# Optimization experiments

Hardware: AMD Instinct MI355X
Metric: run time of the kernel (lower is better)

## Reference

```python
import jax, jax.numpy as jnp
import numpy as np

NUM_HEADS = 12
EPS = 1e-5


def _pool_norm(t, w, g, b, thw, stride):
    # t: [B, heads, 1+L, hd]. Depthwise Conv3d pooling on non-cls tokens, then LayerNorm(hd).
    B, Hn, _, hd = t.shape
    cls, body = t[:, :, :1], t[:, :, 1:]
    T, Hs, Ws = thw
    x = body.reshape(B * Hn, T, Hs, Ws, hd).transpose(0, 4, 1, 2, 3)  # [B*heads, hd, T, H, W]
    pad = [(w.shape[2] // 2,) * 2, (w.shape[3] // 2,) * 2, (w.shape[4] // 2,) * 2]
    y = jax.lax.conv_general_dilated(x, w, window_strides=stride, padding=pad,
                                     feature_group_count=hd,
                                     dimension_numbers=('NCDHW', 'OIDHW', 'NCDHW'))
    Tp, Hp, Wp = y.shape[2], y.shape[3], y.shape[4]
    y = y.reshape(B, Hn, hd, Tp * Hp * Wp).transpose(0, 1, 3, 2)  # [B, heads, Lp, hd]
    y = jnp.concatenate([cls, y], axis=2)
    mu = y.mean(-1, keepdims=True)
    var = ((y - mu) ** 2).mean(-1, keepdims=True)
    return (y - mu) * jax.lax.rsqrt(var + EPS) * g + b


def _forward(x, Wq, Wk, Wv, Wproj, b_proj, pq, pk, pv, gq, bq, gk, bk, gv, bv, thw):
    B, N, C = x.shape
    hd = C // NUM_HEADS
    def proj(W):
        return (x @ W.T).reshape(B, N, NUM_HEADS, hd).transpose(0, 2, 1, 3)  # [B, heads, N, hd]
    q = _pool_norm(proj(Wq), pq, gq, bq, thw, (1, 2, 2))
    k = _pool_norm(proj(Wk), pk, gk, bk, thw, (1, 4, 4))
    v = _pool_norm(proj(Wv), pv, gv, bv, thw, (1, 4, 4))
    scale = hd ** -0.5
    attn = jax.nn.softmax(jnp.einsum('bhqd,bhkd->bhqk', q * scale, k), axis=-1)
    o = jnp.einsum('bhqk,bhkd->bhqd', attn, v)
    o = o.transpose(0, 2, 1, 3).reshape(B, o.shape[2], C)
    return o @ Wproj.T + b_proj


def setup_inputs() -> dict:
    key = jax.random.key(0)
    ks = jax.random.split(key, 8)
    B, T, H, W, C = 8, 8, 28, 28, 768
    hd = C // NUM_HEADS
    N = T * H * W + 1  # cls token
    s = lambda k, sh: jax.random.normal(k, sh, jnp.float32) * 0.02
    return {
        'x': jax.random.normal(ks[0], (B, N, C), jnp.float32),
        'Wq': s(ks[1], (C, C)), 'Wk': s(ks[2], (C, C)), 'Wv': s(ks[3], (C, C)),
        'Wproj': s(ks[4], (C, C)), 'b_proj': jnp.zeros((C,), jnp.float32),
        'pool_q_w': s(ks[5], (hd, 1, 3, 3, 3)),
        'pool_k_w': s(ks[6], (hd, 1, 3, 3, 3)),
        'pool_v_w': s(ks[7], (hd, 1, 3, 3, 3)),
        'gq': jnp.ones((hd,), jnp.float32), 'bq': jnp.zeros((hd,), jnp.float32),
        'gk': jnp.ones((hd,), jnp.float32), 'bk': jnp.zeros((hd,), jnp.float32),
        'gv': jnp.ones((hd,), jnp.float32), 'bv': jnp.zeros((hd,), jnp.float32),
        'thw_t': 8, 'thw_h': 28, 'thw_w': 28,
    }


def reference(x, Wq, Wk, Wv, Wproj, b_proj, pool_q_w, pool_k_w, pool_v_w,
              gq, bq, gk, bk, gv, bv, thw_t, thw_h, thw_w):
    return _forward(x, Wq, Wk, Wv, Wproj, b_proj, pool_q_w, pool_k_w, pool_v_w,
                    gq, bq, gk, bk, gv, bv, (thw_t, thw_h, thw_w))
```

## Files before the change

kernel.cpp:

```cpp
#include <hip/hip_runtime.h>

using bf16   = __bf16;
using bf16x4 = __attribute__((ext_vector_type(4))) __bf16;
using bf16x8 = __attribute__((ext_vector_type(8))) __bf16;
using f32x4  = __attribute__((ext_vector_type(4))) float;
using u32x4  = __attribute__((ext_vector_type(4))) unsigned int;

#define MFMA16(a,b,c) __builtin_amdgcn_mfma_f32_16x16x32_bf16((a),(b),(c),0,0,0)

__device__ inline void glds16(const void* g, void* l) {
    __builtin_amdgcn_global_load_lds(
        (__attribute__((address_space(1))) void*)(const_cast<void*>(g)),
        (__attribute__((address_space(3))) void*)(l), 16, 0, 0);
}

__device__ inline int xcd_remap(int bid, int nwg) {
    const int xcd = bid & 7, loc = bid >> 3;
    const int q8 = nwg >> 3, r8 = nwg & 7;
    return (xcd < r8 ? xcd * (q8 + 1) : r8 * (q8 + 1) + (xcd - r8) * q8) + loc;
}

constexpr int CB   = 8;
constexpr int NH   = 12;
constexpr int CC   = 768;
constexpr int HD   = 64;
constexpr int TT   = 8, HH = 28, WW = 28;
constexpr int NTOK = TT*HH*WW + 1;
constexpr int MX   = CB*NTOK;
constexpr int MXP  = 50304;
constexpr int NQ   = 1569, NQP = 1600;
constexpr int NK   = 393,  NKP = 416;
constexpr int MO   = CB*NQ;
constexpr int MOP  = 12672;
constexpr int CTOK = 1 + TT*20*20;
constexpr int MKV  = CB*CTOK;
constexpr int MKVP = 25856;

__global__ __launch_bounds__(256) void prep_all(const float* __restrict__ x,
                                                const float* __restrict__ Wq, const float* __restrict__ Wk,
                                                const float* __restrict__ Wv, const float* __restrict__ Wp,
                                                const float* __restrict__ pqw, const float* __restrict__ pkw,
                                                const float* __restrict__ pvw,
                                                const float* __restrict__ gq, const float* __restrict__ bq,
                                                const float* __restrict__ gk, const float* __restrict__ bk,
                                                bf16* __restrict__ xb, bf16* __restrict__ wdst,
                                                float* __restrict__ wt, float* __restrict__ Mb) {
    constexpr int WSZ = 589824;
    const int bid = blockIdx.x, tid = threadIdx.x;
    if (bid < 4096) {
        const int nvalid = MX * CC, ntotal = MXP * CC;
        int i = (bid * 256 + tid) * 4;
        const int stride = 4096 * 256 * 4;
        for (; i < ntotal; i += stride) {
            bf16x4 o;
            if (i + 3 < nvalid) {
                f32x4 v = *(const f32x4*)(x + i);
                #pragma unroll
                for (int e = 0; e < 4; ++e) o[e] = (bf16)v[e];
            } else {
                #pragma unroll
                for (int e = 0; e < 4; ++e) {
                    int k = i + e;
                    o[e] = (bf16)((k < nvalid) ? x[k] : 0.f);
                }
            }
            *(bf16x4*)(xb + i) = o;
        }
    } else if (bid < 6400) {
        int i = ((bid - 4096) * 256 + tid) * 4;
        const int setn = i / WSZ, j = i % WSZ;
        const float* src = (setn == 0) ? Wq : (setn == 1) ? Wk : (setn == 2) ? Wv : Wp;
        f32x4 v = *(const f32x4*)(src + j);
        bf16x4 o;
        #pragma unroll
        for (int e = 0; e < 4; ++e) o[e] = (bf16)v[e];
        *(bf16x4*)(wdst + i) = o;
    } else if (bid < 6421) {
        int i = (bid - 6400) * 256 + tid;
        if (i < 3 * 1728) {
            int setn = i / 1728, j = i % 1728;
            const float* src = (setn == 0) ? pqw : (setn == 1) ? pkw : pvw;
            int tap = j / 64, c = j % 64;
            wt[i] = src[c * 27 + tap];
        }
    } else if (tid < 64) {
        const int c = tid;
        float mgq = fabsf(gq[c]), sbq = bq[c] * bq[c];
        float mgk = fabsf(gk[c]), sbk = bk[c] * bk[c];
        #pragma unroll
        for (int m = 1; m < 64; m <<= 1) {
            mgq = fmaxf(mgq, __shfl_xor(mgq, m)); sbq += __shfl_xor(sbq, m);
            mgk = fmaxf(mgk, __shfl_xor(mgk, m)); sbk += __shfl_xor(sbk, m);
        }
        if (c == 0) {
            const float Bq = 8.f * mgq + sqrtf(sbq);
            const float Bk = 8.f * mgk + sqrtf(sbk);
            Mb[0] = 0.125f * Bq * Bk;
        }
    }
}

__global__ __launch_bounds__(512, 2) void gemmU(const bf16* __restrict__ xb,
                                                const bf16* __restrict__ wqkv,
                                                bf16* __restrict__ tmpq,
                                                bf16* __restrict__ tmpkv) {
    extern __shared__ char lds[];
    const int wgid = xcd_remap(blockIdx.x, gridDim.x);

    const int tid = threadIdx.x, lane = tid & 63, w = tid >> 6;
    const int li = lane & 15, lg = lane >> 4;
    const int wr = w >> 2, wc = w & 3;
    const int lr  = lane >> 3;
    const int lsw = ((lane & 7) ^ lr) << 3;

    const bool isQ = wgid < 591;
    int bm, bn, Mv, ldc;
    const bf16* Bb;
    bf16* C;
    if (isQ) { bm = wgid / 3;        bn = wgid % 3;        Mv = MXP;  ldc = 768;
               Bb = wqkv + (size_t)bn * 256 * 768;               C = tmpq; }
    else     { int t = wgid - 591;   bm = t / 6; bn = t % 6; Mv = MKVP; ldc = 1536;
               Bb = wqkv + (size_t)(768 + bn * 256) * 768;       C = tmpkv; }

    const bf16* abase[4];
    const bf16* bbase[4];
    #pragma unroll
    for (int h_ = 0; h_ < 4; ++h_) {
        int gr = bm * 256 + h_ * 64 + w * 8 + lr;
        size_t orig;
        if (isQ) {
            if (gr > MXP - 1) gr = MXP - 1;
            orig = (size_t)gr;
        } else {
            if (gr > MKV - 1) gr = MKV - 1;
            const unsigned b = (unsigned)gr / 3201u;
            const unsigned p = (unsigned)gr % 3201u;
            if (p == 0) orig = (size_t)b * NTOK;
            else {
                const unsigned q  = p - 1;
                const unsigned t2 = q / 400u, rem = q % 400u;
                const unsigned hi = rem / 20u, wi = rem % 20u;
                const int ih = 4 * (int)((hi + 1) / 3) + (int)((hi + 1) % 3) - 1;
                const int iw = 4 * (int)((wi + 1) / 3) + (int)((wi + 1) % 3) - 1;
                orig = (size_t)b * NTOK + 1 + ((size_t)t2 * HH + ih) * WW + iw;
            }
        }
        abase[h_] = xb + orig * 768 + lsw;
        bbase[h_] = Bb + (size_t)(h_ * 64 + w * 8 + lr) * 768 + lsw;
    }

    const int sw_  = (li & 7) << 4;
    const int swc0 = (lg * 16) ^ sw_;
    const int swc1 = (64 | (lg * 16)) ^ sw_;

#define STAGE_T(Tt, buf) do {                                                        \
        char* d_ = lds + (buf) * 65536;                                              \
        _Pragma("unroll")                                                            \
        for (int h_ = 0; h_ < 4; ++h_)                                               \
            glds16(abase[h_] + (size_t)(Tt) * 64, d_ + (h_ * 64 + w * 8) * 128);     \
        _Pragma("unroll")                                                            \
        for (int h_ = 0; h_ < 4; ++h_)                                               \
            glds16(bbase[h_] + (size_t)(Tt) * 64, d_ + 32768 + (h_ * 64 + w * 8) * 128); \
    } while (0)

    f32x4 acc[8][4] = {};
    bf16x8 aF[8], bF[4];

#define READ_K(sw)                                                                   \
    _Pragma("unroll") for (int mf = 0; mf < 8; ++mf)                                 \
        aF[mf] = *(const bf16x8*)(bufA + (size_t)(wr * 128 + mf * 16 + li) * 128 + (sw)); \
    _Pragma("unroll") for (int nf = 0; nf < 4; ++nf)                                 \
        bF[nf] = *(const bf16x8*)(bufB + (size_t)(wc * 64 + nf * 16 + li) * 128 + (sw));

#define MFMA_K()                                                                     \
    _Pragma("unroll") for (int mf = 0; mf < 8; ++mf)                                 \
    _Pragma("unroll") for (int nf = 0; nf < 4; ++nf)                                 \
        acc[mf][nf] = MFMA16(aF[mf], bF[nf], acc[mf][nf]);

    STAGE_T(0, 0);
    STAGE_T(1, 1);
    asm volatile("s_waitcnt vmcnt(8)" ::: "memory");
    __builtin_amdgcn_s_barrier();
    __builtin_amdgcn_sched_barrier(0);

    #pragma unroll
    for (int T = 0; T < 12; ++T) {
        const char* bufA = lds + (T & 1) * 65536;
        const char* bufB = bufA + 32768;
        if (T >= 1 && T < 11) STAGE_T(T + 1, (T + 1) & 1);
        READ_K(swc0);
        __builtin_amdgcn_s_setprio(1);
        MFMA_K();
        __builtin_amdgcn_s_setprio(0);
        READ_K(swc1);
        __builtin_amdgcn_s_setprio(1);
        MFMA_K();
        __builtin_amdgcn_s_setprio(0);
        asm volatile("s_waitcnt lgkmcnt(0)" ::: "memory");
        if (T < 11) asm volatile("s_waitcnt vmcnt(0)" ::: "memory");
        __builtin_amdgcn_s_barrier();
        __builtin_amdgcn_sched_barrier(0);
    }
#undef STAGE_T
#undef READ_K
#undef MFMA_K

    #pragma unroll
    for (int mf = 0; mf < 8; ++mf) {
        const int row0 = bm * 256 + wr * 128 + mf * 16 + lg * 4;
        #pragma unroll
        for (int nf = 0; nf < 4; ++nf) {
            const int col = bn * 256 + wc * 64 + nf * 16 + li;
            #pragma unroll
            for (int r = 0; r < 4; ++r) {
                const int row = row0 + r;
                if (row < Mv)
                    C[(size_t)row * ldc + col] = (bf16)acc[mf][nf][r];
            }
        }
    }
}

__global__ __launch_bounds__(512, 2) void gemmF(const bf16* __restrict__ A,
                                                const bf16* __restrict__ Bw,
                                                float* __restrict__ Cptr,
                                                const float* __restrict__ bias,
                                                int nbn, int Mvalid, int Aclamp) {
    extern __shared__ char lds[];
    const int wgid = xcd_remap(blockIdx.x, gridDim.x);
    const int bm = wgid / nbn, bn = wgid % nbn;

    const int tid = threadIdx.x, lane = tid & 63, w = tid >> 6;
    const int li = lane & 15, lg = lane >> 4;
    const int wr = w >> 2, wc = w & 3;
    const int lr  = lane >> 3;
    const int lsw = ((lane & 7) ^ lr) << 3;
    const bf16* Agp = A  + (size_t)bm * 256 * 768;
    const bf16* Bgp = Bw + (size_t)bn * 128 * 768;
    const int clampA = Aclamp - bm * 256;

    const int sw_  = (li & 7) << 4;
    const int swc0 = (lg * 16) ^ sw_;
    const int swc1 = (64 | (lg * 16)) ^ sw_;

#define STAGE_T(Tt, buf) do {                                                        \
        char* d_ = lds + (buf) * 49152;                                              \
        _Pragma("unroll")                                                            \
        for (int h_ = 0; h_ < 4; ++h_) {                                             \
            const int r0_ = h_ * 64 + w * 8;                                         \
            int gr_ = r0_ + lr; if (gr_ >= clampA) gr_ = clampA - 1;                 \
            glds16(Agp + (size_t)gr_ * 768 + (Tt) * 64 + lsw, d_ + r0_ * 128);       \
        }                                                                            \
        _Pragma("unroll")                                                            \
        for (int h_ = 0; h_ < 2; ++h_) {                                             \
            const int r0_ = h_ * 64 + w * 8;                                         \
            glds16(Bgp + (size_t)(r0_ + lr) * 768 + (Tt) * 64 + lsw,                 \
                   d_ + 32768 + r0_ * 128);                                          \
        } } while (0)

    f32x4 acc[8][2] = {};
    bf16x8 aF[8], bF[2];

#define READ_K(sw)                                                                   \
    _Pragma("unroll") for (int mf = 0; mf < 8; ++mf)                                 \
        aF[mf] = *(const bf16x8*)(bufA + (size_t)(wr * 128 + mf * 16 + li) * 128 + (sw)); \
    _Pragma("unroll") for (int nf = 0; nf < 2; ++nf)                                 \
        bF[nf] = *(const bf16x8*)(bufB + (size_t)(wc * 32 + nf * 16 + li) * 128 + (sw));

#define MFMA_K()                                                                     \
    _Pragma("unroll") for (int mf = 0; mf < 8; ++mf)                                 \
    _Pragma("unroll") for (int nf = 0; nf < 2; ++nf)                                 \
        acc[mf][nf] = MFMA16(aF[mf], bF[nf], acc[mf][nf]);

    STAGE_T(0, 0);
    STAGE_T(1, 1);
    asm volatile("s_waitcnt vmcnt(6)" ::: "memory");
    __builtin_amdgcn_s_barrier();
    __builtin_amdgcn_sched_barrier(0);

    #pragma unroll
    for (int T = 0; T < 12; ++T) {
        const char* bufA = lds + (T & 1) * 49152;
        const char* bufB = bufA + 32768;
        if (T >= 1 && T < 11) STAGE_T(T + 1, (T + 1) & 1);
        READ_K(swc0);
        __builtin_amdgcn_s_setprio(1);
        MFMA_K();
        __builtin_amdgcn_s_setprio(0);
        READ_K(swc1);
        __builtin_amdgcn_s_setprio(1);
        MFMA_K();
        __builtin_amdgcn_s_setprio(0);
        asm volatile("s_waitcnt lgkmcnt(0)" ::: "memory");
        if (T < 11) asm volatile("s_waitcnt vmcnt(0)" ::: "memory");
        __builtin_amdgcn_s_barrier();
        __builtin_amdgcn_sched_barrier(0);
    }
#undef STAGE_T
#undef READ_K
#undef MFMA_K

    #pragma unroll
    for (int mf = 0; mf < 8; ++mf) {
        const int row0 = bm * 256 + wr * 128 + mf * 16 + lg * 4;
        #pragma unroll
        for (int nf = 0; nf < 2; ++nf) {
            const int col = bn * 128 + wc * 32 + nf * 16 + li;
            #pragma unroll
            for (int r = 0; r < 4; ++r) {
                const int row = row0 + r;
                if (row < Mvalid)
                    Cptr[(size_t)row * 768 + col] = acc[mf][nf][r] + bias[col];
            }
        }
    }
}

__device__ __forceinline__ void pool_q4(int gw, int lane,
                                        const bf16* __restrict__ P,
                                        const float* __restrict__ wt,
                                        const float* __restrict__ gamma,
                                        const float* __restrict__ beta,
                                        bf16* __restrict__ outp) {
    constexpr int TASKS = 57;
    const int bh = gw / TASKS, task = gw % TASKS;
    const int b = bh / NH, head = bh % NH;
    const int owp = lane >> 3, cg = lane & 7, c = cg * 8;
    const size_t pbase = (size_t)b * NTOK * 768 + head * HD + c;

    if (task == TASKS - 1) {
        if (owp == 0) {
            bf16x8 v = *(const bf16x8*)(P + pbase);
            float a[8];
            #pragma unroll
            for (int e = 0; e < 8; ++e) a[e] = (float)v[e];
            float s = 0;
            #pragma unroll
            for (int e = 0; e < 8; ++e) s += a[e];
            s += __shfl_xor(s, 1); s += __shfl_xor(s, 2); s += __shfl_xor(s, 4);
            const float mu = s * 0.015625f;
            float v2 = 0;
            #pragma unroll
            for (int e = 0; e < 8; ++e) { float d = a[e] - mu; v2 += d * d; }
            v2 += __shfl_xor(v2, 1); v2 += __shfl_xor(v2, 2); v2 += __shfl_xor(v2, 4);
            const float rs = rsqrtf(v2 * 0.015625f + 1e-5f);
            f32x4 g0 = *(const f32x4*)(gamma + c), g1 = *(const f32x4*)(gamma + c + 4);
            f32x4 b0 = *(const f32x4*)(beta + c),  b1 = *(const f32x4*)(beta + c + 4);
            bf16x8 o;
            #pragma unroll
            for (int e = 0; e < 4; ++e) {
                o[e]     = (bf16)(((a[e]     - mu) * rs * g0[e] + b0[e]) * 0.125f);
                o[4 + e] = (bf16)(((a[4 + e] - mu) * rs * g1[e] + b1[e]) * 0.125f);
            }
            *(bf16x8*)(outp + ((size_t)bh * NQP) * HD + c) = o;
        } else {
            bf16x8 z = {};
            for (int p = NQ + owp - 1; p < NQP; p += 7)
                *(bf16x8*)(outp + ((size_t)bh * NQP + p) * HD + c) = z;
        }
        return;
    }

    const int tp = task / 14, oh = task % 14;
    const bool active = (owp < 7);

    float a00[8] = {}, a01[8] = {}, a10[8] = {}, a11[8] = {};
    #pragma unroll
    for (int pl = 0; pl < 4; ++pl) {
        const int it = 2 * tp - 1 + pl;
        if (it < 0 || it >= TT) continue;
        #pragma unroll
        for (int dh = 0; dh < 3; ++dh) {
            const int ih = 2 * oh + dh - 1;
            if (ih < 0 || ih >= HH) continue;
            const int rowh = 1 + (it * HH + ih) * WW;
            #pragma unroll
            for (int du = 0; du < 5; ++du) {
                const int iw = 4 * owp - 1 + du;
                if (active && iw >= 0 && iw < WW) {
                    bf16x8 v = *(const bf16x8*)(P + pbase + (size_t)(rowh + iw) * 768);
                    float fv[8];
                    #pragma unroll
                    for (int e = 0; e < 8; ++e) fv[e] = (float)v[e];
#define TAP(ACC, DT, DW) do {                                                        \
        const float* wp_ = wt + (((DT) * 3 + dh) * 3 + (DW)) * 64 + c;               \
        f32x4 w0_ = *(const f32x4*)wp_, w1_ = *(const f32x4*)(wp_ + 4);              \
        _Pragma("unroll")                                                            \
        for (int e = 0; e < 4; ++e) {                                                \
            ACC[e]     += w0_[e] * fv[e];                                            \
            ACC[4 + e] += w1_[e] * fv[4 + e];                                        \
        } } while (0)
                    if (du <= 2) {
                        if (pl <= 2) TAP(a00, pl,     du);
                        if (pl >= 1) TAP(a10, pl - 1, du);
                    }
                    if (du >= 2) {
                        if (pl <= 2) TAP(a01, pl,     du - 2);
                        if (pl >= 1) TAP(a11, pl - 1, du - 2);
                    }
#undef TAP
                }
            }
        }
    }
    f32x4 g0 = *(const f32x4*)(gamma + c), g1 = *(const f32x4*)(gamma + c + 4);
    f32x4 b0 = *(const f32x4*)(beta + c),  b1 = *(const f32x4*)(beta + c + 4);
#define LNSTORE(ACC, HT, HW) do {                                                    \
        float s_ = 0;                                                                \
        _Pragma("unroll") for (int e = 0; e < 8; ++e) s_ += ACC[e];                  \
        s_ += __shfl_xor(s_, 1); s_ += __shfl_xor(s_, 2); s_ += __shfl_xor(s_, 4);   \
        const float mu_ = s_ * 0.015625f;                                            \
        float v2_ = 0;                                                               \
        _Pragma("unroll") for (int e = 0; e < 8; ++e) {                              \
            float d_ = ACC[e] - mu_; v2_ += d_ * d_; }                               \
        v2_ += __shfl_xor(v2_, 1); v2_ += __shfl_xor(v2_, 2); v2_ += __shfl_xor(v2_, 4); \
        const float rs_ = rsqrtf(v2_ * 0.015625f + 1e-5f);                           \
        if (active) {                                                                \
            bf16x8 o_;                                                               \
            _Pragma("unroll") for (int e = 0; e < 4; ++e) {                          \
                o_[e]     = (bf16)(((ACC[e]     - mu_) * rs_ * g0[e] + b0[e]) * 0.125f); \
                o_[4 + e] = (bf16)(((ACC[4 + e] - mu_) * rs_ * g1[e] + b1[e]) * 0.125f); \
            }                                                                        \
            const int p_ = 1 + ((2 * tp + (HT)) * 14 + oh) * 14 + (2 * owp + (HW));  \
            *(bf16x8*)(outp + ((size_t)bh * NQP + p_) * HD + c) = o_;                \
        } } while (0)
    LNSTORE(a00, 0, 0);
    LNSTORE(a01, 0, 1);
    LNSTORE(a10, 1, 0);
    LNSTORE(a11, 1, 1);
#undef LNSTORE
}

template<int S, int OH, int OW, int CH, int NP, int NPpad, int SRCSTRIDE, bool COMPACT>
__device__ __forceinline__ void pool_body2(int gw, int lane,
                                           const bf16* __restrict__ P,
                                           const float* __restrict__ wt,
                                           const float* __restrict__ gamma,
                                           const float* __restrict__ beta,
                                           bf16* __restrict__ outp,
                                           float outScale) {
    constexpr int TASKS = 4 * OH * CH + 1;
    const int bh = gw / TASKS, task = gw % TASKS;
    const int b = bh / NH, head = bh % NH;
    const int owg = lane >> 3, cg = lane & 7, c = cg * 8;
    const size_t rowbase = COMPACT ? (size_t)b * CTOK : (size_t)b * NTOK;
    const size_t pbase = rowbase * SRCSTRIDE + head * HD + c;

    if (task == TASKS - 1) {
        if (owg == 0) {
            bf16x8 v = *(const bf16x8*)(P + pbase);
            float a[8];
            #pragma unroll
            for (int e = 0; e < 8; ++e) a[e] = (float)v[e];
            float s = 0;
            #pragma unroll
            for (int e = 0; e < 8; ++e) s += a[e];
            s += __shfl_xor(s, 1); s += __shfl_xor(s, 2); s += __shfl_xor(s, 4);
            const float mu = s * 0.015625f;
            float v2 = 0;
            #pragma unroll
            for (int e = 0; e < 8; ++e) { float d = a[e] - mu; v2 += d * d; }
            v2 += __shfl_xor(v2, 1); v2 += __shfl_xor(v2, 2); v2 += __shfl_xor(v2, 4);
            const float rs = rsqrtf(v2 * 0.015625f + 1e-5f);
            f32x4 g0 = *(const f32x4*)(gamma + c), g1 = *(const f32x4*)(gamma + c + 4);
            f32x4 b0 = *(const f32x4*)(beta + c),  b1 = *(const f32x4*)(beta + c + 4);
            bf16x8 o;
            #pragma unroll
            for (int e = 0; e < 4; ++e) {
                o[e]     = (bf16)(((a[e]     - mu) * rs * g0[e] + b0[e]) * outScale);
                o[4 + e] = (bf16)(((a[4 + e] - mu) * rs * g1[e] + b1[e]) * outScale);
            }
            *(bf16x8*)(outp + ((size_t)bh * NPpad) * HD + c) = o;
        } else {
            bf16x8 z = {};
            for (int p = NP + owg - 1; p < NPpad; p += 7)
                *(bf16x8*)(outp + ((size_t)bh * NPpad + p) * HD + c) = z;
        }
        return;
    }

    const int tp = task / (OH * CH);
    const int r2 = task % (OH * CH);
    const int oh = r2 / CH;
    const int ow = (r2 % CH) * 8 + owg;
    const bool active = (ow < OW);

    float acc0[8] = {}, acc1[8] = {};
    #pragma unroll
    for (int pl = 0; pl < 4; ++pl) {
        const int it = 2 * tp - 1 + pl;
        if (it < 0 || it >= TT) continue;
        #pragma unroll
        for (int dh = 0; dh < 3; ++dh) {
            int rowh;
            if constexpr (COMPACT) {
                const int hi = 3 * oh + dh - 1;
                if (hi < 0) continue;
                rowh = 1 + it * 400 + hi * 20;
            } else {
                const int ih = oh * S + dh - 1;
                if (ih < 0 || ih >= HH) continue;
                rowh = 1 + (it * HH + ih) * WW;
            }
            #pragma unroll
            for (int dw = 0; dw < 3; ++dw) {
                int rowoff;
                bool ok;
                if constexpr (COMPACT) {
                    const int wi = 3 * ow + dw - 1;
                    ok = active && (wi >= 0);
                    rowoff = rowh + wi;
                } else {
                    const int iw = ow * S + dw - 1;
                    ok = active && (iw >= 0);
                    rowoff = rowh + iw;
                }
                if (ok) {
                    bf16x8 v = *(const bf16x8*)(P + pbase + (size_t)rowoff * SRCSTRIDE);
                    float fv[8];
                    #pragma unroll
                    for (int e = 0; e < 8; ++e) fv[e] = (float)v[e];
                    if (pl <= 2) {
                        const float* wp = wt + ((pl * 3 + dh) * 3 + dw) * 64 + c;
                        f32x4 w0 = *(const f32x4*)wp, w1 = *(const f32x4*)(wp + 4);
                        #pragma unroll
                        for (int e = 0; e < 4; ++e) {
                            acc0[e]     += w0[e] * fv[e];
                            acc0[4 + e] += w1[e] * fv[4 + e];
                        }
                    }
                    if (pl >= 1) {
                        const float* wp = wt + (((pl - 1) * 3 + dh) * 3 + dw) * 64 + c;
                        f32x4 w0 = *(const f32x4*)wp, w1 = *(const f32x4*)(wp + 4);
                        #pragma unroll
                        for (int e = 0; e < 4; ++e) {
                            acc1[e]     += w0[e] * fv[e];
                            acc1[4 + e] += w1[e] * fv[4 + e];
                        }
                    }
                }
            }
        }
    }
    f32x4 g0 = *(const f32x4*)(gamma + c), g1 = *(const f32x4*)(gamma + c + 4);
    f32x4 b0 = *(const f32x4*)(beta + c),  b1 = *(const f32x4*)(beta + c + 4);
    #pragma unroll
    for (int half = 0; half < 2; ++half) {
        float* acc = half ? acc1 : acc0;
        float s = 0;
        #pragma unroll
        for (int e = 0; e < 8; ++e) s += acc[e];
        s += __shfl_xor(s, 1); s += __shfl_xor(s, 2); s += __shfl_xor(s, 4);
        const float mu = s * 0.015625f;
        float v2 = 0;
        #pragma unroll
        for (int e = 0; e < 8; ++e) { float d = acc[e] - mu; v2 += d * d; }
        v2 += __shfl_xor(v2, 1); v2 += __shfl_xor(v2, 2); v2 += __shfl_xor(v2, 4);
        const float rs = rsqrtf(v2 * 0.015625f + 1e-5f);
        if (active) {
            bf16x8 o;
            #pragma unroll
            for (int e = 0; e < 4; ++e) {
                o[e]     = (bf16)(((acc[e]     - mu) * rs * g0[e] + b0[e]) * outScale);
                o[4 + e] = (bf16)(((acc[4 + e] - mu) * rs * g1[e] + b1[e]) * outScale);
            }
            const int p = 1 + ((2 * tp + half) * OH + oh) * OW + ow;
            *(bf16x8*)(outp + ((size_t)bh * NPpad + p) * HD + c) = o;
        }
    }
}

__global__ __launch_bounds__(256) void pools_all(const bf16* __restrict__ tmpq,
                                                 const bf16* __restrict__ tmpkv,
                                                 const float* __restrict__ wt,
                                                 const float* __restrict__ gq, const float* __restrict__ bq,
                                                 const float* __restrict__ gk, const float* __restrict__ bk,
                                                 const float* __restrict__ gv, const float* __restrict__ bv,
                                                 bf16* __restrict__ qn, bf16* __restrict__ kn,
                                                 bf16* __restrict__ vnb) {
    const int w = threadIdx.x >> 6, lane = threadIdx.x & 63;
    const int bid = blockIdx.x;
    if (bid < 1368) {
        const int gw = xcd_remap(bid, 1368) * 4 + w;
        pool_q4(gw, lane, tmpq, wt, gq, bq, qn);
    } else if (bid < 2064) {
        const int gw = xcd_remap(bid - 1368, 696) * 4 + w;
        pool_body2<4, 7, 7, 1, NK, NKP, 1536, true>(gw, lane, tmpkv, wt + 1728, gk, bk, kn, 1.0f);
    } else {
        const int gw = xcd_remap(bid - 2064, 696) * 4 + w;
        pool_body2<4, 7, 7, 1, NK, NKP, 1536, true>(gw, lane, tmpkv + 768, wt + 3456, gv, bv, vnb, 1.0f);
    }
}

__global__ __launch_bounds__(256) void attn_kernel(const bf16* __restrict__ qn,
                                                   const bf16* __restrict__ kn,
                                                   const bf16* __restrict__ vn,
                                                   bf16* __restrict__ ob,
                                                   const float* __restrict__ Mptr) {
    __shared__ bf16 Kl[2][32][72];
    __shared__ bf16 Vt[2][64][40];
    __shared__ bf16 Pl[4][16][40];

    const int tid = threadIdx.x, l = tid & 63, w = tid >> 6;
    const int li = l & 15, lg = l >> 4;
    const int wgid = xcd_remap(blockIdx.x, gridDim.x);
    const int bh = wgid / 25;
    const int b = bh / NH, head = bh % NH;
    const int qbase = (wgid % 25) * 64 + w * 16;
    const float M = Mptr[0];

    const bf16* qp = qn + ((size_t)bh * NQP + qbase + li) * HD + lg * 8;
    const bf16x8 aq0 = *(const bf16x8*)qp;
    const bf16x8 aq1 = *(const bf16x8*)(qp + 32);

    const int srow = tid >> 3, scol = (tid & 7) * 8;
    const int sj = tid & 31, sd8 = tid >> 5;
    const bf16* kbase = kn + (size_t)bh * NKP * HD;
    const bf16* vbase = vn + (size_t)bh * NKP * HD;

    u32x4 kv = *(const u32x4*)(kbase + srow * HD + scol);
    u32x4 vv = *(const u32x4*)(vbase + sj * HD + sd8 * 8);
    *(u32x4*)&Kl[0][srow][scol] = kv;
    {
        bf16x8 t = __builtin_bit_cast(bf16x8, vv);
        #pragma unroll
        for (int e = 0; e < 8; ++e) Vt[0][sd8 * 8 + e][sj] = t[e];
    }

    f32x4 oacc[4] = {};
    float lpart[4] = {0.f, 0.f, 0.f, 0.f};

    for (int kt = 0; kt < 13; ++kt) {
        const int cur = kt & 1;
        if (kt < 12) {
            kv = *(const u32x4*)(kbase + (kt + 1) * 32 * HD + srow * HD + scol);
            vv = *(const u32x4*)(vbase + (kt + 1) * 32 * HD + sj * HD + sd8 * 8);
        }
        __syncthreads();

        f32x4 c0 = {}, c1 = {};
        const bf16x8 b00 = *(const bf16x8*)&Kl[cur][li][lg * 8];
        const bf16x8 b01 = *(const bf16x8*)&Kl[cur][li][32 + lg * 8];
        const bf16x8 b10 = *(const bf16x8*)&Kl[cur][16 + li][lg * 8];
        const bf16x8 b11 = *(const bf16x8*)&Kl[cur][16 + li][32 + lg * 8];
        __builtin_amdgcn_s_setprio(1);
        c0 = MFMA16(aq0, b00, c0); c0 = MFMA16(aq1, b01, c0);
        c1 = MFMA16(aq0, b10, c1); c1 = MFMA16(aq1, b11, c1);
        __builtin_amdgcn_s_setprio(0);

        float p0[4], p1[4];
        #pragma unroll
        for (int r = 0; r < 4; ++r) {
            p0[r] = __expf(c0[r] - M);
            p1[r] = __expf(c1[r] - M);
        }
        if (kt == 12) {
            const bool m0 = (384 + li) >= NK;
            #pragma unroll
            for (int r = 0; r < 4; ++r) { if (m0) p0[r] = 0.f; p1[r] = 0.f; }
        }
        #pragma unroll
        for (int r = 0; r < 4; ++r) {
            lpart[r] += p0[r] + p1[r];
            Pl[w][lg * 4 + r][li]      = (bf16)p0[r];
            Pl[w][lg * 4 + r][16 + li] = (bf16)p1[r];
        }
        const bf16x8 ap = *(const bf16x8*)&Pl[w][li][lg * 8];
        __builtin_amdgcn_s_setprio(1);
        #pragma unroll
        for (int dg = 0; dg < 4; ++dg) {
            const bf16x8 bv = *(const bf16x8*)&Vt[cur][dg * 16 + li][lg * 8];
            oacc[dg] = MFMA16(ap, bv, oacc[dg]);
        }
        __builtin_amdgcn_s_setprio(0);

        if (kt < 12) {
            const int nxt = cur ^ 1;
            *(u32x4*)&Kl[nxt][srow][scol] = kv;
            bf16x8 t = __builtin_bit_cast(bf16x8, vv);
            #pragma unroll
            for (int e = 0; e < 8; ++e) Vt[nxt][sd8 * 8 + e][sj] = t[e];
        }
    }
    #pragma unroll
    for (int r = 0; r < 4; ++r) {
        float lsum = lpart[r];
        lsum += __shfl_xor(lsum, 1);
        lsum += __shfl_xor(lsum, 2);
        lsum += __shfl_xor(lsum, 4);
        lsum += __shfl_xor(lsum, 8);
        const int q = qbase + lg * 4 + r;
        if (q < NQ) {
            const float inv = 1.f / lsum;
            const size_t off = ((size_t)(b * NQ + q)) * CC + head * HD;
            #pragma unroll
            for (int dg = 0; dg < 4; ++dg)
                ob[off + dg * 16 + li] = (bf16)(oacc[dg][r] * inv);
        }
    }
}

extern "C" void kernel_launch(void* const* d_in, const int* in_sizes, int n_in,
                              void* d_out, int out_size, void* d_ws, size_t ws_size,
                              hipStream_t stream) {
    const float* x     = (const float*)d_in[0];
    const float* Wq    = (const float*)d_in[1];
    const float* Wk    = (const float*)d_in[2];
    const float* Wv    = (const float*)d_in[3];
    const float* Wproj = (const float*)d_in[4];
    const float* bproj = (const float*)d_in[5];
    const float* pqw   = (const float*)d_in[6];
    const float* pkw   = (const float*)d_in[7];
    const float* pvw   = (const float*)d_in[8];
    const float* gq    = (const float*)d_in[9];
    const float* bq    = (const float*)d_in[10];
    const float* gk    = (const float*)d_in[11];
    const float* bk    = (const float*)d_in[12];
    const float* gv    = (const float*)d_in[13];
    const float* bv    = (const float*)d_in[14];

    if (ws_size < 364000000ULL) return;
    char* ws = (char*)d_ws;
    bf16* xb    = (bf16*)(ws);
    bf16* wqkv  = (bf16*)(ws + 77266944);
    bf16* wpb   = (bf16*)(ws + 80805888);
    bf16* tmpq  = (bf16*)(ws + 81985536);
    bf16* tmpkv = (bf16*)(ws + 159252480);
    bf16* qn    = (bf16*)(ws + 238682112);
    bf16* kn    = (bf16*)(ws + 258342912);
    bf16* vnb   = (bf16*)(ws + 263454720);
    bf16* ob    = (bf16*)(ws + 268566528);
    float* wt   = (float*)(ws + 288030720);
    float* Mb   = (float*)(ws + 288051456);

    (void)hipFuncSetAttribute((const void*)gemmU,
                              hipFuncAttributeMaxDynamicSharedMemorySize, 131072);
    (void)hipFuncSetAttribute((const void*)gemmF,
                              hipFuncAttributeMaxDynamicSharedMemorySize, 98304);

    prep_all<<<6422, 256, 0, stream>>>(x, Wq, Wk, Wv, Wproj, pqw, pkw, pvw,
                                       gq, bq, gk, bk, xb, wqkv, wt, Mb);

    gemmU<<<1197, 512, 131072, stream>>>(xb, wqkv, tmpq, tmpkv);

    pools_all<<<2760, 256, 0, stream>>>(tmpq, tmpkv, wt, gq, bq, gk, bk, gv, bv,
                                        qn, kn, vnb);

    attn_kernel<<<2400, 256, 0, stream>>>(qn, kn, vnb, ob, Mb);

    gemmF<<<50 * 6, 512, 98304, stream>>>(ob, wpb, (float*)d_out, bproj, 6, MO, MOP);
}
```

Before: 323.4 us.

## Process two query tiles per wave in attention to reuse K/V LDS tiles

Each wave now handles 32 query rows (two 16-row MFMA fragments) instead of 16, so each block covers 128 queries and the grid shrinks by roughly half. K and V tiles staged in LDS are reused across twice as many queries, halving global K/V loads and LDS staging work per query. Query padding grows to 1664 and workspace offsets shift to fit. The cost is more registers per thread and fewer blocks, which may reduce occupancy and latency hiding.

```diff
diff --git a/kernel.cpp b/kernel.cpp
--- a/kernel.cpp
+++ b/kernel.cpp
@@ -28,7 +28,7 @@
 constexpr int NTOK = TT*HH*WW + 1;
 constexpr int MX   = CB*NTOK;
 constexpr int MXP  = 50304;
-constexpr int NQ   = 1569, NQP = 1600;
+constexpr int NQ   = 1569, NQP = 1664;
 constexpr int NK   = 393,  NKP = 416;
 constexpr int MO   = CB*NQ;
 constexpr int MOP  = 12672;
@@ -599,19 +599,23 @@
                                                    const float* __restrict__ Mptr) {
     __shared__ bf16 Kl[2][32][72];
     __shared__ bf16 Vt[2][64][40];
-    __shared__ bf16 Pl[4][16][40];
+    __shared__ bf16 Pl[4][32][40];
 
     const int tid = threadIdx.x, l = tid & 63, w = tid >> 6;
     const int li = l & 15, lg = l >> 4;
     const int wgid = xcd_remap(blockIdx.x, gridDim.x);
-    const int bh = wgid / 25;
+    const int bh = wgid / 13;
     const int b = bh / NH, head = bh % NH;
-    const int qbase = (wgid % 25) * 64 + w * 16;
+    const int qbase = (wgid % 13) * 128 + w * 32;
     const float M = Mptr[0];
 
-    const bf16* qp = qn + ((size_t)bh * NQP + qbase + li) * HD + lg * 8;
-    const bf16x8 aq0 = *(const bf16x8*)qp;
-    const bf16x8 aq1 = *(const bf16x8*)(qp + 32);
+    bf16x8 aq[2][2];
+    #pragma unroll
+    for (int qf = 0; qf < 2; ++qf) {
+        const bf16* qp = qn + ((size_t)bh * NQP + qbase + qf * 16 + li) * HD + lg * 8;
+        aq[qf][0] = *(const bf16x8*)qp;
+        aq[qf][1] = *(const bf16x8*)(qp + 32);
+    }
 
     const int srow = tid >> 3, scol = (tid & 7) * 8;
     const int sj = tid & 31, sd8 = tid >> 5;
@@ -627,8 +631,8 @@
         for (int e = 0; e < 8; ++e) Vt[0][sd8 * 8 + e][sj] = t[e];
     }
 
-    f32x4 oacc[4] = {};
-    float lpart[4] = {0.f, 0.f, 0.f, 0.f};
+    f32x4 oacc[2][4] = {};
+    float lpart[2][4] = {};
 
     for (int kt = 0; kt < 13; ++kt) {
         const int cur = kt & 1;
@@ -638,39 +642,45 @@
         }
         __syncthreads();
 
-        f32x4 c0 = {}, c1 = {};
         const bf16x8 b00 = *(const bf16x8*)&Kl[cur][li][lg * 8];
         const bf16x8 b01 = *(const bf16x8*)&Kl[cur][li][32 + lg * 8];
         const bf16x8 b10 = *(const bf16x8*)&Kl[cur][16 + li][lg * 8];
         const bf16x8 b11 = *(const bf16x8*)&Kl[cur][16 + li][32 + lg * 8];
-        __builtin_amdgcn_s_setprio(1);
-        c0 = MFMA16(aq0, b00, c0); c0 = MFMA16(aq1, b01, c0);
-        c1 = MFMA16(aq0, b10, c1); c1 = MFMA16(aq1, b11, c1);
-        __builtin_amdgcn_s_setprio(0);
-
-        float p0[4], p1[4];
-        #pragma unroll
-        for (int r = 0; r < 4; ++r) {
-            p0[r] = __expf(c0[r] - M);
-            p1[r] = __expf(c1[r] - M);
-        }
-        if (kt == 12) {
-            const bool m0 = (384 + li) >= NK;
-            #pragma unroll
-            for (int r = 0; r < 4; ++r) { if (m0) p0[r] = 0.f; p1[r] = 0.f; }
-        }
-        #pragma unroll
-        for (int r = 0; r < 4; ++r) {
-            lpart[r] += p0[r] + p1[r];
-            Pl[w][lg * 4 + r][li]      = (bf16)p0[r];
-            Pl[w][lg * 4 + r][16 + li] = (bf16)p1[r];
-        }
-        const bf16x8 ap = *(const bf16x8*)&Pl[w][li][lg * 8];
+
+        #pragma unroll
+        for (int qf = 0; qf < 2; ++qf) {
+            f32x4 c0 = {}, c1 = {};
+            __builtin_amdgcn_s_setprio(1);
+            c0 = MFMA16(aq[qf][0], b00, c0); c0 = MFMA16(aq[qf][1], b01, c0);
+            c1 = MFMA16(aq[qf][0], b10, c1); c1 = MFMA16(aq[qf][1], b11, c1);
+            __builtin_amdgcn_s_setprio(0);
+
+            float p0[4], p1[4];
+            #pragma unroll
+            for (int r = 0; r < 4; ++r) {
+                p0[r] = __expf(c0[r] - M);
+                p1[r] = __expf(c1[r] - M);
+            }
+            if (kt == 12) {
+                const bool m0 = (384 + li) >= NK;
+                #pragma unroll
+                for (int r = 0; r < 4; ++r) { if (m0) p0[r] = 0.f; p1[r] = 0.f; }
+            }
+            #pragma unroll
+            for (int r = 0; r < 4; ++r) {
+                lpart[qf][r] += p0[r] + p1[r];
+                Pl[w][qf * 16 + lg * 4 + r][li]      = (bf16)p0[r];
+                Pl[w][qf * 16 + lg * 4 + r][16 + li] = (bf16)p1[r];
+            }
+        }
+        const bf16x8 ap0 = *(const bf16x8*)&Pl[w][li][lg * 8];
+        const bf16x8 ap1 = *(const bf16x8*)&Pl[w][16 + li][lg * 8];
         __builtin_amdgcn_s_setprio(1);
         #pragma unroll
         for (int dg = 0; dg < 4; ++dg) {
             const bf16x8 bv = *(const bf16x8*)&Vt[cur][dg * 16 + li][lg * 8];
-            oacc[dg] = MFMA16(ap, bv, oacc[dg]);
+            oacc[0][dg] = MFMA16(ap0, bv, oacc[0][dg]);
+            oacc[1][dg] = MFMA16(ap1, bv, oacc[1][dg]);
         }
         __builtin_amdgcn_s_setprio(0);
 
@@ -683,19 +693,22 @@
         }
     }
     #pragma unroll
-    for (int r = 0; r < 4; ++r) {
-        float lsum = lpart[r];
-        lsum += __shfl_xor(lsum, 1);
-        lsum += __shfl_xor(lsum, 2);
-        lsum += __shfl_xor(lsum, 4);
-        lsum += __shfl_xor(lsum, 8);
-        const int q = qbase + lg * 4 + r;
-        if (q < NQ) {
-            const float inv = 1.f / lsum;
-            const size_t off = ((size_t)(b * NQ + q)) * CC + head * HD;
-            #pragma unroll
-            for (int dg = 0; dg < 4; ++dg)
-                ob[off + dg * 16 + li] = (bf16)(oacc[dg][r] * inv);
+    for (int qf = 0; qf < 2; ++qf) {
+        #pragma unroll
+        for (int r = 0; r < 4; ++r) {
+            float lsum = lpart[qf][r];
+            lsum += __shfl_xor(lsum, 1);
+            lsum += __shfl_xor(lsum, 2);
+            lsum += __shfl_xor(lsum, 4);
+            lsum += __shfl_xor(lsum, 8);
+            const int q = qbase + qf * 16 + lg * 4 + r;
+            if (q < NQ) {
+                const float inv = 1.f / lsum;
+                const size_t off = ((size_t)(b * NQ + q)) * CC + head * HD;
+                #pragma unroll
+                for (int dg = 0; dg < 4; ++dg)
+                    ob[off + dg * 16 + li] = (bf16)(oacc[qf][dg][r] * inv);
+            }
         }
     }
 }
@@ -727,11 +740,11 @@
     bf16* tmpq  = (bf16*)(ws + 81985536);
     bf16* tmpkv = (bf16*)(ws + 159252480);
     bf16* qn    = (bf16*)(ws + 238682112);
-    bf16* kn    = (bf16*)(ws + 258342912);
-    bf16* vnb   = (bf16*)(ws + 263454720);
-    bf16* ob    = (bf16*)(ws + 268566528);
-    float* wt   = (float*)(ws + 288030720);
-    float* Mb   = (float*)(ws + 288051456);
+    bf16* kn    = (bf16*)(ws + 259129344);
+    bf16* vnb   = (bf16*)(ws + 264241152);
+    bf16* ob    = (bf16*)(ws + 269352960);
+    float* wt   = (float*)(ws + 288817152);
+    float* Mb   = (float*)(ws + 288837888);
 
     (void)hipFuncSetAttribute((const void*)gemmU,
                               hipFuncAttributeMaxDynamicSharedMemorySize, 131072);
@@ -746,7 +759,7 @@
     pools_all<<<2760, 256, 0, stream>>>(tmpq, tmpkv, wt, gq, bq, gk, bk, gv, bv,
                                         qn, kn, vnb);
 
-    attn_kernel<<<2400, 256, 0, stream>>>(qn, kn, vnb, ob, Mb);
+    attn_kernel<<<1248, 256, 0, stream>>>(qn, kn, vnb, ob, Mb);
 
     gemmF<<<50 * 6, 512, 98304, stream>>>(ob, wpb, (float*)d_out, bproj, 6, MO, MOP);
 }
```

New measurement: 320.0 us. No clear change (-1.0%).
